# Kernel tuning notes

Hardware: AMD Instinct MI355X
Metric: run time of the kernel (lower is better)

The kernel has to match this reference:

```python
import jax, jax.numpy as jnp
import numpy as np

S, H, E, N, K, R, NL, L = 256, 768, 1536, 16, 4, 48, 2, 1024


def setup_inputs() -> dict:
    key = jax.random.key(0)
    ks = jax.random.split(key, 12)
    def rn(k, shape, s=0.02):
        return jax.random.normal(k, shape, jnp.float32) * s
    return {
        "x": jax.random.normal(ks[0], (L, S), jnp.float32),
        "emb_w": rn(ks[1], (H, S)),
        "emb_b": rn(ks[2], (H,)),
        "norm_w": jnp.ones((NL, H), jnp.float32),
        "in_proj_w": rn(ks[3], (NL, 2 * E, H)),
        "conv_w": rn(ks[4], (NL, E, K), 0.1),
        "conv_b": rn(ks[5], (NL, E), 0.1),
        "x_proj_w": rn(ks[6], (NL, R + 2 * N, E)),
        "dt_proj_w": rn(ks[7], (NL, E, R), 0.1),
        "dt_proj_b": rn(ks[8], (NL, E), 0.1),
        "A_log": jnp.log(jnp.tile(jnp.arange(1, N + 1, dtype=jnp.float32), (NL, E, 1))),
        "D": jnp.ones((NL, E), jnp.float32),
        "out_proj_w": rn(ks[9], (NL, H, E)),
        "head_w": rn(ks[10], (S, H)),
        "head_b": rn(ks[11], (S,)),
    }


def rmsnorm(x, w, eps=1e-5):
    return x * jax.lax.rsqrt(jnp.mean(x * x, axis=-1, keepdims=True) + eps) * w


def causal_conv1d(x, w, b):
    # x: (L, E), w: (E, K) depthwise kernel, causal (left-pad K-1)
    xp = jnp.pad(x, ((K - 1, 0), (0, 0)))
    y = sum(w[:, k] * xp[k:k + x.shape[0]] for k in range(K))
    return y + b


def mamba_mixer(x, in_w, cw, cb, xp_w, dt_w, dt_b, a_log, d, out_w):
    xz = x @ in_w.T                       # (L, 2E)
    xin, z = jnp.split(xz, 2, axis=-1)
    u = jax.nn.silu(causal_conv1d(xin, cw, cb))   # (L, E)
    dbc = u @ xp_w.T                      # (L, R+2N)
    dt, B, C = dbc[:, :R], dbc[:, R:R + N], dbc[:, R + N:]
    dt = jax.nn.softplus(dt @ dt_w.T + dt_b)      # (L, E)
    A = -jnp.exp(a_log)                   # (E, N)
    dA = jnp.exp(dt[:, :, None] * A)      # (L, E, N)
    dBu = dt[:, :, None] * B[:, None, :] * u[:, :, None]  # (L, E, N)

    def step(s, t):
        dA_t, dBu_t, C_t = t
        s = s * dA_t + dBu_t              # (E, N)
        return s, s @ C_t                 # y_t: (E,)

    _, ys = jax.lax.scan(step, jnp.zeros((E, N), x.dtype), (dA, dBu, C))
    y = ys + u * d
    return (y * jax.nn.silu(z)) @ out_w.T


def reference(x, emb_w, emb_b, norm_w, in_proj_w, conv_w, conv_b, x_proj_w,
              dt_proj_w, dt_proj_b, A_log, D, out_proj_w, head_w, head_b):
    h = x @ emb_w.T + emb_b               # (L, H)
    res = None
    for i in range(NL):
        res = h if res is None else h + res
        hn = rmsnorm(res, norm_w[i])
        h = mamba_mixer(hn, in_proj_w[i], conv_w[i], conv_b[i], x_proj_w[i],
                        dt_proj_w[i], dt_proj_b[i], A_log[i], D[i], out_proj_w[i])
    return h @ head_w.T + head_b          # (L, S)
```

## Files before the change

### kernel.cpp

```cpp
#include <hip/hip_runtime.h>
#include <hip/hip_bf16.h>
#include <math.h>

#define SDIM 256
#define HDIM 768
#define EDIM 1536
#define NDIM 16
#define KCONV 4
#define RDIM 48
#define NLAYER 2
#define LSEQ 1024

#define NCHUNK 128
#define CHLEN (LSEQ / NCHUNK)
#define XSPLIT 4
#define XKCH (EDIM / XSPLIT)

typedef __hip_bfloat16 bf16;
typedef __attribute__((ext_vector_type(8))) short short8;
typedef __attribute__((ext_vector_type(4))) float f32x4;

__device__ __forceinline__ float softplusf(float x) {
    return (x > 20.f) ? x : log1pf(expf(x));
}
__device__ __forceinline__ float siluf(float x) {
    return x / (1.f + expf(-x));
}

struct F2BSegs {
    const float* src[6];
    bf16*        dst[6];
    int          n[6];
};

__global__ __launch_bounds__(256) void f2b_all(F2BSegs segs)
{
    for (int s = 0; s < 6; s++) {
        const float* __restrict__ in = segs.src[s];
        bf16* __restrict__ out = segs.dst[s];
        const int n = segs.n[s];
        for (int i = (blockIdx.x * 256 + threadIdx.x) * 4; i < n; i += gridDim.x * 256 * 4) {
            float4 v = *(const float4*)(in + i);
            out[i + 0] = (bf16)v.x; out[i + 1] = (bf16)v.y;
            out[i + 2] = (bf16)v.z; out[i + 3] = (bf16)v.w;
        }
    }
}

__global__ __launch_bounds__(256) void k_gemm_sk(const bf16* __restrict__ A, int lda,
                                                 const bf16* __restrict__ W, int ldw,
                                                 const float* __restrict__ bias,
                                                 float* __restrict__ part,
                                                 int N, int Kh, int useBias)
{
    __shared__ __align__(16) short As[64][72];
    __shared__ __align__(16) short Ws[64][72];

    const int tid  = threadIdx.x;
    const int lane = tid & 63, wid = tid >> 6;
    const int wm = wid >> 1, wn = wid & 1;
    const int row0 = blockIdx.y * 64, col0 = blockIdx.x * 64;
    const int quad = lane >> 4, l16 = lane & 15;
    const int kbase = blockIdx.z * Kh;

    f32x4 acc[2][2] = {};
    for (int k0 = 0; k0 < Kh; k0 += 64) {
        #pragma unroll
        for (int i = 0; i < 2; i++) {
            int id = tid + i * 256;
            int r = id >> 3, g = id & 7;
            *(uint4*)&As[r][g * 8] = *(const uint4*)(A + (size_t)(row0 + r) * lda + kbase + k0 + g * 8);
            *(uint4*)&Ws[r][g * 8] = *(const uint4*)(W + (size_t)(col0 + r) * ldw + kbase + k0 + g * 8);
        }
        __syncthreads();
        #pragma unroll
        for (int ks = 0; ks < 64; ks += 32) {
            short8 af[2], bfr[2];
            #pragma unroll
            for (int i = 0; i < 2; i++) af[i] = *(const short8*)&As[wm * 32 + i * 16 + l16][ks + quad * 8];
            #pragma unroll
            for (int j = 0; j < 2; j++) bfr[j] = *(const short8*)&Ws[wn * 32 + j * 16 + l16][ks + quad * 8];
            #pragma unroll
            for (int i = 0; i < 2; i++)
                #pragma unroll
                for (int j = 0; j < 2; j++)
                    acc[i][j] = __builtin_amdgcn_mfma_f32_16x16x32_bf16(af[i], bfr[j], acc[i][j], 0, 0, 0);
        }
        __syncthreads();
    }
    float* pdst = part + (size_t)blockIdx.z * LSEQ * N;
    #pragma unroll
    for (int i = 0; i < 2; i++) {
        #pragma unroll
        for (int j = 0; j < 2; j++) {
            int gn = col0 + wn * 32 + j * 16 + l16;
            int gm0 = row0 + wm * 32 + i * 16 + quad * 4;
            #pragma unroll
            for (int r = 0; r < 4; r++) {
                float v = acc[i][j][r];
                if (useBias && blockIdx.z == 0) v += bias[gn];
                pdst[(size_t)(gm0 + r) * N + gn] = v;
            }
        }
    }
}

__global__ __launch_bounds__(256) void k_gemm_h(const float* __restrict__ A0,
                                                const float* __restrict__ A1, int lda,
                                                const bf16* __restrict__ W, int ldw,
                                                const float* __restrict__ bias,
                                                float* __restrict__ out, int N, int Kd)
{
    __shared__ __align__(16) short As[64][72];
    __shared__ __align__(16) short Ws[64][72];

    const int tid  = threadIdx.x;
    const int lane = tid & 63, wid = tid >> 6;
    const int wm = wid >> 1, wn = wid & 1;
    const int row0 = blockIdx.y * 64, col0 = blockIdx.x * 64;
    const int quad = lane >> 4, l16 = lane & 15;

    f32x4 acc[2][2] = {};
    for (int k0 = 0; k0 < Kd; k0 += 64) {
        #pragma unroll
        for (int i = 0; i < 2; i++) {
            int id = tid + i * 256;
            int r = id >> 3, g = id & 7;
            size_t base = (size_t)(row0 + r) * lda + k0 + g * 8;
            float4 a0 = *(const float4*)(A0 + base);
            float4 a1 = *(const float4*)(A0 + base + 4);
            float4 b0 = *(const float4*)(A1 + base);
            float4 b1 = *(const float4*)(A1 + base + 4);
            bf16 tmp[8] = {(bf16)(a0.x + b0.x), (bf16)(a0.y + b0.y),
                           (bf16)(a0.z + b0.z), (bf16)(a0.w + b0.w),
                           (bf16)(a1.x + b1.x), (bf16)(a1.y + b1.y),
                           (bf16)(a1.z + b1.z), (bf16)(a1.w + b1.w)};
            *(uint4*)&As[r][g * 8] = *(const uint4*)tmp;
            *(uint4*)&Ws[r][g * 8] = *(const uint4*)(W + (size_t)(col0 + r) * ldw + k0 + g * 8);
        }
        __syncthreads();
        #pragma unroll
        for (int ks = 0; ks < 64; ks += 32) {
            short8 af[2], bfr[2];
            #pragma unroll
            for (int i = 0; i < 2; i++) af[i] = *(const short8*)&As[wm * 32 + i * 16 + l16][ks + quad * 8];
            #pragma unroll
            for (int j = 0; j < 2; j++) bfr[j] = *(const short8*)&Ws[wn * 32 + j * 16 + l16][ks + quad * 8];
            #pragma unroll
            for (int i = 0; i < 2; i++)
                #pragma unroll
                for (int j = 0; j < 2; j++)
                    acc[i][j] = __builtin_amdgcn_mfma_f32_16x16x32_bf16(af[i], bfr[j], acc[i][j], 0, 0, 0);
        }
        __syncthreads();
    }
    #pragma unroll
    for (int i = 0; i < 2; i++) {
        #pragma unroll
        for (int j = 0; j < 2; j++) {
            int gn = col0 + wn * 32 + j * 16 + l16;
            int gm0 = row0 + wm * 32 + i * 16 + quad * 4;
            #pragma unroll
            for (int r = 0; r < 4; r++)
                out[(size_t)(gm0 + r) * N + gn] = acc[i][j][r] + bias[gn];
        }
    }
}

__global__ __launch_bounds__(256) void k_gemm128(
    const bf16* __restrict__ A, int lda,
    const bf16* __restrict__ W, int ldw,
    float* __restrict__ out, int N, int Kd)
{
    __shared__ __align__(16) short As[128][64];
    __shared__ __align__(16) short Ws[128][64];

    const int tid  = threadIdx.x;
    const int lane = tid & 63, wid = tid >> 6;
    const int wm = wid >> 1, wn = wid & 1;
    const int row0 = blockIdx.y * 128, col0 = blockIdx.x * 128;
    const int quad = lane >> 4, l16 = lane & 15;
    const int lr = lane >> 3;
    const int lk = ((lane & 7) ^ lr) * 8;

    f32x4 acc[4][4] = {};

    for (int k0 = 0; k0 < Kd; k0 += 64) {
        #pragma unroll
        for (int j = 0; j < 4; j++) {
            int rg = (wid * 4 + j) * 8;
            const bf16* ga = A + (size_t)(row0 + rg + lr) * lda + k0 + lk;
            const bf16* gw = W + (size_t)(col0 + rg + lr) * ldw + k0 + lk;
            __builtin_amdgcn_global_load_lds(
                (const __attribute__((address_space(1))) void*)ga,
                (__attribute__((address_space(3))) void*)&As[rg][0], 16, 0, 0);
            __builtin_amdgcn_global_load_lds(
                (const __attribute__((address_space(1))) void*)gw,
                (__attribute__((address_space(3))) void*)&Ws[rg][0], 16, 0, 0);
        }
        __syncthreads();

        #pragma unroll
        for (int ks = 0; ks < 64; ks += 32) {
            const int g = (ks >> 3) + quad;
            short8 af[4], bfr[4];
            #pragma unroll
            for (int i = 0; i < 4; i++) {
                int r = wm * 64 + i * 16 + l16;
                af[i] = *(const short8*)&As[r][(g ^ (r & 7)) * 8];
            }
            #pragma unroll
            for (int j = 0; j < 4; j++) {
                int r = wn * 64 + j * 16 + l16;
                bfr[j] = *(const short8*)&Ws[r][(g ^ (r & 7)) * 8];
            }
            #pragma unroll
            for (int i = 0; i < 4; i++)
                #pragma unroll
                for (int j = 0; j < 4; j++)
                    acc[i][j] = __builtin_amdgcn_mfma_f32_16x16x32_bf16(af[i], bfr[j], acc[i][j], 0, 0, 0);
        }
        __syncthreads();
    }

    #pragma unroll
    for (int i = 0; i < 4; i++) {
        #pragma unroll
        for (int j = 0; j < 4; j++) {
            int gn = col0 + wn * 64 + j * 16 + l16;
            int gm0 = row0 + wm * 64 + i * 16 + quad * 4;
            #pragma unroll
            for (int r = 0; r < 4; r++)
                out[(size_t)(gm0 + r) * N + gn] = acc[i][j][r];
        }
    }
}

__global__ __launch_bounds__(256) void k_conv(const float* __restrict__ xz,
                                              const float* __restrict__ cw,
                                              const float* __restrict__ cb,
                                              float* __restrict__ u,
                                              bf16* __restrict__ ub)
{
    const int NG = LSEQ * EDIM / 4;
    for (int g = blockIdx.x * 256 + threadIdx.x; g < NG; g += gridDim.x * 256) {
        int t = g / (EDIM / 4);
        int e4 = (g - t * (EDIM / 4)) * 4;
        float4 s = *(const float4*)(cb + e4);
        #pragma unroll
        for (int k = 0; k < KCONV; k++) {
            int tt = t - (KCONV - 1) + k;
            if (tt >= 0) {
                float4 xv = *(const float4*)(xz + (size_t)tt * (2 * EDIM) + e4);
                s.x += cw[(e4 + 0) * KCONV + k] * xv.x;
                s.y += cw[(e4 + 1) * KCONV + k] * xv.y;
                s.z += cw[(e4 + 2) * KCONV + k] * xv.z;
                s.w += cw[(e4 + 3) * KCONV + k] * xv.w;
            }
        }
        float4 uv;
        uv.x = siluf(s.x); uv.y = siluf(s.y); uv.z = siluf(s.z); uv.w = siluf(s.w);
        size_t o = (size_t)t * EDIM + e4;
        *(float4*)(u + o) = uv;
        bf16 tmp[4] = {(bf16)uv.x, (bf16)uv.y, (bf16)uv.z, (bf16)uv.w};
        *(uint2*)(ub + o) = *(const uint2*)tmp;
    }
}

__global__ __launch_bounds__(256) void k_xproj_mfma(
    const bf16* __restrict__ A,
    const bf16* __restrict__ W,
    float* __restrict__ part)
{
    __shared__ __align__(16) short As[64][72];
    __shared__ __align__(16) short Ws[64][72];

    const int tid  = threadIdx.x;
    const int lane = tid & 63, wid = tid >> 6;
    const int wm = wid >> 1, wn = wid & 1;
    const int row0 = blockIdx.y * 64, col0 = blockIdx.x * 64;
    const int quad = lane >> 4, l16 = lane & 15;
    const int kbase = blockIdx.z * XKCH;

    f32x4 acc[2][2] = {};
    for (int k0 = 0; k0 < XKCH; k0 += 64) {
        #pragma unroll
        for (int i = 0; i < 2; i++) {
            int id = tid + i * 256;
            int r = id >> 3, g = id & 7;
            *(uint4*)&As[r][g * 8] =
                *(const uint4*)(A + (size_t)(row0 + r) * EDIM + kbase + k0 + g * 8);
            uint4 wv = {0, 0, 0, 0};
            if (col0 + r < 80)
                wv = *(const uint4*)(W + (size_t)(col0 + r) * EDIM + kbase + k0 + g * 8);
            *(uint4*)&Ws[r][g * 8] = wv;
        }
        __syncthreads();
        #pragma unroll
        for (int ks = 0; ks < 64; ks += 32) {
            short8 af[2], bfr[2];
            #pragma unroll
            for (int i = 0; i < 2; i++) af[i] = *(const short8*)&As[wm * 32 + i * 16 + l16][ks + quad * 8];
            #pragma unroll
            for (int j = 0; j < 2; j++) bfr[j] = *(const short8*)&Ws[wn * 32 + j * 16 + l16][ks + quad * 8];
            #pragma unroll
            for (int i = 0; i < 2; i++)
                #pragma unroll
                for (int j = 0; j < 2; j++)
                    acc[i][j] = __builtin_amdgcn_mfma_f32_16x16x32_bf16(af[i], bfr[j], acc[i][j], 0, 0, 0);
        }
        __syncthreads();
    }

    float* pdst = part + (size_t)blockIdx.z * (LSEQ * 80);
    #pragma unroll
    for (int i = 0; i < 2; i++) {
        #pragma unroll
        for (int j = 0; j < 2; j++) {
            int gn = col0 + wn * 32 + j * 16 + l16;
            int gm0 = row0 + wm * 32 + i * 16 + quad * 4;
            if (gn < 80) {
                #pragma unroll
                for (int r = 0; r < 4; r++)
                    pdst[(size_t)(gm0 + r) * 80 + gn] = acc[i][j][r];
            }
        }
    }
}

__global__ __launch_bounds__(256) void k_dt_red(
    const float* __restrict__ part, const float* __restrict__ dtw,
    const float* __restrict__ dtbb, float* __restrict__ out,
    float* __restrict__ dbc)
{
    __shared__ float AsF[16][68];
    __shared__ float WsF[16][68];
    const int tid = threadIdx.x;
    const int tx = tid & 15, ty = tid >> 4;
    const int tx4 = tx * 4, ty4 = ty * 4;
    const int row0 = blockIdx.y * 64, col0 = blockIdx.x * 64;

    if (blockIdx.x == 0) {
        for (int idx = tid; idx < 64 * 32; idx += 256) {
            int m = idx >> 5, c = 48 + (idx & 31);
            size_t o = (size_t)(row0 + m) * 80 + c;
            float s = 0.f;
            #pragma unroll
            for (int p = 0; p < XSPLIT; p++) s += part[(size_t)p * (LSEQ * 80) + o];
            dbc[o] = s;
        }
    }

    float acc[4][4] = {};
    for (int k0 = 0; k0 < RDIM; k0 += 16) {
        #pragma unroll
        for (int i = 0; i < 4; i++) {
            int idx = tid + i * 256;
            int m = idx >> 4, kk = idx & 15;
            size_t o = (size_t)(row0 + m) * 80 + k0 + kk;
            float s = 0.f;
            #pragma unroll
            for (int p = 0; p < XSPLIT; p++) s += part[(size_t)p * (LSEQ * 80) + o];
            AsF[kk][m] = s;
        }
        #pragma unroll
        for (int i = 0; i < 4; i++) {
            int idx = tid + i * 256;
            int nn = idx >> 4, kk = idx & 15;
            WsF[kk][nn] = dtw[(size_t)(col0 + nn) * RDIM + k0 + kk];
        }
        __syncthreads();
        #pragma unroll
        for (int kk = 0; kk < 16; kk++) {
            float av[4], bv[4];
            #pragma unroll
            for (int i = 0; i < 4; i++) av[i] = AsF[kk][ty4 + i];
            #pragma unroll
            for (int j = 0; j < 4; j++) bv[j] = WsF[kk][tx4 + j];
            #pragma unroll
            for (int i = 0; i < 4; i++)
                #pragma unroll
                for (int j = 0; j < 4; j++)
                    acc[i][j] += av[i] * bv[j];
        }
        __syncthreads();
    }
    #pragma unroll
    for (int i = 0; i < 4; i++) {
        int gm = row0 + ty4 + i;
        #pragma unroll
        for (int j = 0; j < 4; j++) {
            int gn = col0 + tx4 + j;
            float v = acc[i][j] + dtbb[gn];
            out[(size_t)gm * EDIM + gn] = softplusf(v);
        }
    }
}

__global__ __launch_bounds__(256) void k_rms(const float* __restrict__ h0,
                                             const float* __restrict__ h1,
                                             float* __restrict__ res,
                                             bf16* __restrict__ hnb, const float* __restrict__ w,
                                             int first)
{
    __shared__ float red[4];
    __shared__ float tot;
    const int tid = threadIdx.x;
    const int t = blockIdx.x;
    float v[3]; float ss = 0.f;
    #pragma unroll
    for (int r = 0; r < 3; r++) {
        int j = tid + r * 256;
        float xv = h0[(size_t)t * HDIM + j] + h1[(size_t)t * HDIM + j];
        if (!first) xv += res[(size_t)t * HDIM + j];
        v[r] = xv;
        res[(size_t)t * HDIM + j] = xv;
        ss += xv * xv;
    }
    #pragma unroll
    for (int m = 32; m >= 1; m >>= 1) ss += __shfl_down(ss, m);
    int wid = tid >> 6;
    if ((tid & 63) == 0) red[wid] = ss;
    __syncthreads();
    if (tid == 0) tot = red[0] + red[1] + red[2] + red[3];
    __syncthreads();
    float scale = rsqrtf(tot / (float)HDIM + 1e-5f);
    #pragma unroll
    for (int r = 0; r < 3; r++) {
        int j = tid + r * 256;
        hnb[(size_t)t * HDIM + j] = (bf16)(v[r] * scale * w[j]);
    }
}

__global__ __launch_bounds__(256) void k_scan1(const float* __restrict__ dt,
                                               const float* __restrict__ u,
                                               const float* __restrict__ dbc,
                                               const float* __restrict__ a_log,
                                               float* __restrict__ chunkS,
                                               float* __restrict__ sumdt)
{
    const int ex = blockIdx.x % 6, c = blockIdx.x / 6;
    const int e = ex * 256 + threadIdx.x;
    float A[16];
    #pragma unroll
    for (int q = 0; q < 4; q++) {
        float4 a4 = *(const float4*)(a_log + e * NDIM + q * 4);
        A[q*4+0] = -__expf(a4.x); A[q*4+1] = -__expf(a4.y);
        A[q*4+2] = -__expf(a4.z); A[q*4+3] = -__expf(a4.w);
    }
    float s[16] = {};
    float sd = 0.f;
    const int t0 = c * CHLEN;
    #pragma unroll
    for (int tt = 0; tt < CHLEN; tt++) {
        int t = t0 + tt;
        float dtv = dt[(size_t)t * EDIM + e];
        float uv  = u[(size_t)t * EDIM + e];
        float dtu = dtv * uv;
        sd += dtv;
        float4 B4[4];
        #pragma unroll
        for (int q = 0; q < 4; q++) B4[q] = *(const float4*)(dbc + (size_t)t * 80 + RDIM + q * 4);
        const float* B = (const float*)B4;
        #pragma unroll
        for (int n = 0; n < 16; n++) s[n] = s[n] * __expf(dtv * A[n]) + dtu * B[n];
    }
    float* cs = chunkS + ((size_t)c * EDIM + e) * NDIM;
    #pragma unroll
    for (int q = 0; q < 4; q++)
        *(float4*)(cs + q * 4) = make_float4(s[q*4+0], s[q*4+1], s[q*4+2], s[q*4+3]);
    sumdt[(size_t)c * EDIM + e] = sd;
}

__global__ __launch_bounds__(256) void k_scan2(const float* __restrict__ chunkS,
                                               const float* __restrict__ sumdt,
                                               const float* __restrict__ a_log,
                                               float* __restrict__ sInit)
{
    int gid = blockIdx.x * 256 + threadIdx.x;
    if (gid >= EDIM * NDIM) return;
    int n = gid & 15, e = gid >> 4;
    const float Aen = -__expf(a_log[gid]);
    float s = 0.f;
    for (int c = 0; c < NCHUNK; c++) {
        sInit[((size_t)c * EDIM + e) * NDIM + n] = s;
        float P = __expf(Aen * sumdt[(size_t)c * EDIM + e]);
        s = s * P + chunkS[((size_t)c * EDIM + e) * NDIM + n];
    }
}

__global__ __launch_bounds__(256) void k_scan3(const float* __restrict__ dt,
                                               const float* __restrict__ u,
                                               const float* __restrict__ dbc,
                                               const float* __restrict__ xz,
                                               const float* __restrict__ a_log,
                                               const float* __restrict__ Dp,
                                               const float* __restrict__ sInit,
                                               bf16* __restrict__ yzb)
{
    const int ex = blockIdx.x % 6, c = blockIdx.x / 6;
    const int e = ex * 256 + threadIdx.x;
    float A[16];
    #pragma unroll
    for (int q = 0; q < 4; q++) {
        float4 a4 = *(const float4*)(a_log + e * NDIM + q * 4);
        A[q*4+0] = -__expf(a4.x); A[q*4+1] = -__expf(a4.y);
        A[q*4+2] = -__expf(a4.z); A[q*4+3] = -__expf(a4.w);
    }
    const float dv = Dp[e];
    float s[16];
    const float* si = sInit + ((size_t)c * EDIM + e) * NDIM;
    #pragma unroll
    for (int q = 0; q < 4; q++) {
        float4 s4 = *(const float4*)(si + q * 4);
        s[q*4+0] = s4.x; s[q*4+1] = s4.y; s[q*4+2] = s4.z; s[q*4+3] = s4.w;
    }
    const int t0 = c * CHLEN;
    #pragma unroll
    for (int tt = 0; tt < CHLEN; tt++) {
        int t = t0 + tt;
        float dtv = dt[(size_t)t * EDIM + e];
        float uv  = u[(size_t)t * EDIM + e];
        float zv  = xz[(size_t)t * (2 * EDIM) + EDIM + e];
        float dtu = dtv * uv;
        float4 B4[4], C4[4];
        #pragma unroll
        for (int q = 0; q < 4; q++) {
            B4[q] = *(const float4*)(dbc + (size_t)t * 80 + RDIM + q * 4);
            C4[q] = *(const float4*)(dbc + (size_t)t * 80 + RDIM + NDIM + q * 4);
        }
        const float* B = (const float*)B4;
        const float* C = (const float*)C4;
        float y = 0.f;
        #pragma unroll
        for (int n = 0; n < 16; n++) {
            s[n] = s[n] * __expf(dtv * A[n]) + dtu * B[n];
            y += s[n] * C[n];
        }
        y += uv * dv;
        yzb[(size_t)t * EDIM + e] = (bf16)(y * siluf(zv));
    }
}

extern "C" void kernel_launch(void* const* d_in, const int* in_sizes, int n_in,
                              void* d_out, int out_size, void* d_ws, size_t ws_size,
                              hipStream_t stream)
{
    const float* x        = (const float*)d_in[0];
    const float* emb_w    = (const float*)d_in[1];
    const float* emb_b    = (const float*)d_in[2];
    const float* norm_w   = (const float*)d_in[3];
    const float* in_proj  = (const float*)d_in[4];
    const float* conv_w   = (const float*)d_in[5];
    const float* conv_b   = (const float*)d_in[6];
    const float* x_proj   = (const float*)d_in[7];
    const float* dt_w     = (const float*)d_in[8];
    const float* dt_b     = (const float*)d_in[9];
    const float* A_log    = (const float*)d_in[10];
    const float* Dp       = (const float*)d_in[11];
    const float* out_proj = (const float*)d_in[12];
    const float* head_w   = (const float*)d_in[13];
    const float* head_b   = (const float*)d_in[14];
    float* out = (float*)d_out;

    float* ws = (float*)d_ws;
    size_t off = 0;
    float* hpart  = ws + off; off += (size_t)2 * LSEQ * HDIM;
    float* res    = ws + off; off += (size_t)LSEQ * HDIM;
    float* xz     = ws + off; off += (size_t)LSEQ * 2 * EDIM;
    float* u      = ws + off; off += (size_t)LSEQ * EDIM;
    float* dbc    = ws + off; off += (size_t)LSEQ * 80;
    float* part   = ws + off; off += (size_t)XSPLIT * LSEQ * 80;
    float* dtb    = ws + off; off += (size_t)LSEQ * EDIM;
    float* chunkS = ws + off; off += (size_t)NCHUNK * EDIM * NDIM;
    float* sumdt  = ws + off; off += (size_t)NCHUNK * EDIM;
    float* sInit  = ws + off; off += (size_t)NCHUNK * EDIM * NDIM;
    bf16* hnb     = (bf16*)(ws + off); off += (size_t)LSEQ * HDIM / 2;
    bf16* yzb     = (bf16*)(ws + off); off += (size_t)LSEQ * EDIM / 2;
    bf16* ub      = (bf16*)(ws + off); off += (size_t)LSEQ * EDIM / 2;
    bf16* xb      = (bf16*)(ws + off); off += (size_t)LSEQ * SDIM / 2;
    bf16* emb_wb  = (bf16*)(ws + off); off += (size_t)HDIM * SDIM / 2;
    bf16* head_wb = (bf16*)(ws + off); off += (size_t)SDIM * HDIM / 2;
    bf16* in_wb   = (bf16*)(ws + off); off += (size_t)NLAYER * 2 * EDIM * HDIM / 2;
    bf16* out_wb  = (bf16*)(ws + off); off += (size_t)NLAYER * HDIM * EDIM / 2;
    bf16* xwb     = (bf16*)(ws + off); off += (size_t)NLAYER * 80 * EDIM / 2;

    F2BSegs segs;
    segs.src[0] = x;        segs.dst[0] = xb;      segs.n[0] = LSEQ * SDIM;
    segs.src[1] = emb_w;    segs.dst[1] = emb_wb;  segs.n[1] = HDIM * SDIM;
    segs.src[2] = head_w;   segs.dst[2] = head_wb; segs.n[2] = SDIM * HDIM;
    segs.src[3] = in_proj;  segs.dst[3] = in_wb;   segs.n[3] = NLAYER * 2 * EDIM * HDIM;
    segs.src[4] = out_proj; segs.dst[4] = out_wb;  segs.n[4] = NLAYER * HDIM * EDIM;
    segs.src[5] = x_proj;   segs.dst[5] = xwb;     segs.n[5] = NLAYER * 80 * EDIM;
    f2b_all<<<1024, 256, 0, stream>>>(segs);

    k_gemm_sk<<<dim3(12, 16, 2), 256, 0, stream>>>(xb, SDIM, emb_wb, SDIM, emb_b,
                                                   hpart, HDIM, SDIM / 2, 1);

    for (int l = 0; l < NLAYER; l++) {
        const bf16*  inw  = in_wb  + (size_t)l * 2 * EDIM * HDIM;
        const bf16*  outw = out_wb + (size_t)l * HDIM * EDIM;
        const bf16*  xwbl = xwb    + (size_t)l * 80 * EDIM;
        const float* cw   = conv_w + (size_t)l * EDIM * KCONV;
        const float* cb   = conv_b + (size_t)l * EDIM;
        const float* dtw  = dt_w   + (size_t)l * EDIM * RDIM;
        const float* dtbb = dt_b   + (size_t)l * EDIM;
        const float* al   = A_log  + (size_t)l * EDIM * NDIM;
        const float* Dpl  = Dp     + (size_t)l * EDIM;

        k_rms<<<LSEQ, 256, 0, stream>>>(hpart, hpart + (size_t)LSEQ * HDIM, res,
                                        hnb, norm_w + (size_t)l * HDIM, l == 0);
        k_gemm128<<<dim3(24, 8), 256, 0, stream>>>(hnb, HDIM, inw, HDIM,
                                                   xz, 2 * EDIM, HDIM);
        k_conv<<<1536, 256, 0, stream>>>(xz, cw, cb, u, ub);
        k_xproj_mfma<<<dim3(2, 16, XSPLIT), 256, 0, stream>>>(ub, xwbl, part);
        k_dt_red<<<dim3(24, 16), 256, 0, stream>>>(part, dtw, dtbb, dtb, dbc);
        k_scan1<<<6 * NCHUNK, 256, 0, stream>>>(dtb, u, dbc, al, chunkS, sumdt);
        k_scan2<<<96, 256, 0, stream>>>(chunkS, sumdt, al, sInit);
        k_scan3<<<6 * NCHUNK, 256, 0, stream>>>(dtb, u, dbc, xz, al, Dpl, sInit, yzb);
        k_gemm_sk<<<dim3(12, 16, 2), 256, 0, stream>>>(yzb, EDIM, outw, EDIM, nullptr,
                                                       hpart, HDIM, EDIM / 2, 0);
    }

    k_gemm_h<<<dim3(4, 16), 256, 0, stream>>>(hpart, hpart + (size_t)LSEQ * HDIM, HDIM,
                                              head_wb, HDIM, head_b, out, SDIM, HDIM);
}
```

Before: 375.7 us.

## Split-K in_proj GEMM, drop fp32 u buffer, halve scan chunk count

The dedicated 128x128 in_proj GEMM is replaced by the split-K GEMM kernel. It writes two partial xz buffers, which the conv and scan3 kernels sum when they read them. The fp32 u activation is no longer stored, and the scans read the bf16 copy instead, cutting memory traffic at some cost in precision. The scan chunk count drops from 128 to 64 with partial unrolling, which reduces chunk-state traffic but lengthens each serial chunk.

```diff
diff --git a/kernel.cpp b/kernel.cpp
--- a/kernel.cpp
+++ b/kernel.cpp
@@ -11,7 +11,7 @@
 #define NLAYER 2
 #define LSEQ 1024
 
-#define NCHUNK 128
+#define NCHUNK 64
 #define CHLEN (LSEQ / NCHUNK)
 #define XSPLIT 4
 #define XKCH (EDIM / XSPLIT)
@@ -167,79 +167,10 @@
     }
 }
 
-__global__ __launch_bounds__(256) void k_gemm128(
-    const bf16* __restrict__ A, int lda,
-    const bf16* __restrict__ W, int ldw,
-    float* __restrict__ out, int N, int Kd)
-{
-    __shared__ __align__(16) short As[128][64];
-    __shared__ __align__(16) short Ws[128][64];
-
-    const int tid  = threadIdx.x;
-    const int lane = tid & 63, wid = tid >> 6;
-    const int wm = wid >> 1, wn = wid & 1;
-    const int row0 = blockIdx.y * 128, col0 = blockIdx.x * 128;
-    const int quad = lane >> 4, l16 = lane & 15;
-    const int lr = lane >> 3;
-    const int lk = ((lane & 7) ^ lr) * 8;
-
-    f32x4 acc[4][4] = {};
-
-    for (int k0 = 0; k0 < Kd; k0 += 64) {
-        #pragma unroll
-        for (int j = 0; j < 4; j++) {
-            int rg = (wid * 4 + j) * 8;
-            const bf16* ga = A + (size_t)(row0 + rg + lr) * lda + k0 + lk;
-            const bf16* gw = W + (size_t)(col0 + rg + lr) * ldw + k0 + lk;
-            __builtin_amdgcn_global_load_lds(
-                (const __attribute__((address_space(1))) void*)ga,
-                (__attribute__((address_space(3))) void*)&As[rg][0], 16, 0, 0);
-            __builtin_amdgcn_global_load_lds(
-                (const __attribute__((address_space(1))) void*)gw,
-                (__attribute__((address_space(3))) void*)&Ws[rg][0], 16, 0, 0);
-        }
-        __syncthreads();
-
-        #pragma unroll
-        for (int ks = 0; ks < 64; ks += 32) {
-            const int g = (ks >> 3) + quad;
-            short8 af[4], bfr[4];
-            #pragma unroll
-            for (int i = 0; i < 4; i++) {
-                int r = wm * 64 + i * 16 + l16;
-                af[i] = *(const short8*)&As[r][(g ^ (r & 7)) * 8];
-            }
-            #pragma unroll
-            for (int j = 0; j < 4; j++) {
-                int r = wn * 64 + j * 16 + l16;
-                bfr[j] = *(const short8*)&Ws[r][(g ^ (r & 7)) * 8];
-            }
-            #pragma unroll
-            for (int i = 0; i < 4; i++)
-                #pragma unroll
-                for (int j = 0; j < 4; j++)
-                    acc[i][j] = __builtin_amdgcn_mfma_f32_16x16x32_bf16(af[i], bfr[j], acc[i][j], 0, 0, 0);
-        }
-        __syncthreads();
-    }
-
-    #pragma unroll
-    for (int i = 0; i < 4; i++) {
-        #pragma unroll
-        for (int j = 0; j < 4; j++) {
-            int gn = col0 + wn * 64 + j * 16 + l16;
-            int gm0 = row0 + wm * 64 + i * 16 + quad * 4;
-            #pragma unroll
-            for (int r = 0; r < 4; r++)
-                out[(size_t)(gm0 + r) * N + gn] = acc[i][j][r];
-        }
-    }
-}
-
-__global__ __launch_bounds__(256) void k_conv(const float* __restrict__ xz,
+__global__ __launch_bounds__(256) void k_conv(const float* __restrict__ xzp0,
+                                              const float* __restrict__ xzp1,
                                               const float* __restrict__ cw,
                                               const float* __restrict__ cb,
-                                              float* __restrict__ u,
                                               bf16* __restrict__ ub)
 {
     const int NG = LSEQ * EDIM / 4;
@@ -251,19 +182,17 @@
         for (int k = 0; k < KCONV; k++) {
             int tt = t - (KCONV - 1) + k;
             if (tt >= 0) {
-                float4 xv = *(const float4*)(xz + (size_t)tt * (2 * EDIM) + e4);
-                s.x += cw[(e4 + 0) * KCONV + k] * xv.x;
-                s.y += cw[(e4 + 1) * KCONV + k] * xv.y;
-                s.z += cw[(e4 + 2) * KCONV + k] * xv.z;
-                s.w += cw[(e4 + 3) * KCONV + k] * xv.w;
+                size_t o = (size_t)tt * (2 * EDIM) + e4;
+                float4 xa = *(const float4*)(xzp0 + o);
+                float4 xb2 = *(const float4*)(xzp1 + o);
+                s.x += cw[(e4 + 0) * KCONV + k] * (xa.x + xb2.x);
+                s.y += cw[(e4 + 1) * KCONV + k] * (xa.y + xb2.y);
+                s.z += cw[(e4 + 2) * KCONV + k] * (xa.z + xb2.z);
+                s.w += cw[(e4 + 3) * KCONV + k] * (xa.w + xb2.w);
             }
         }
-        float4 uv;
-        uv.x = siluf(s.x); uv.y = siluf(s.y); uv.z = siluf(s.z); uv.w = siluf(s.w);
-        size_t o = (size_t)t * EDIM + e4;
-        *(float4*)(u + o) = uv;
-        bf16 tmp[4] = {(bf16)uv.x, (bf16)uv.y, (bf16)uv.z, (bf16)uv.w};
-        *(uint2*)(ub + o) = *(const uint2*)tmp;
+        bf16 tmp[4] = {(bf16)siluf(s.x), (bf16)siluf(s.y), (bf16)siluf(s.z), (bf16)siluf(s.w)};
+        *(uint2*)(ub + (size_t)t * EDIM + e4) = *(const uint2*)tmp;
     }
 }
 
@@ -433,7 +362,7 @@
 }
 
 __global__ __launch_bounds__(256) void k_scan1(const float* __restrict__ dt,
-                                               const float* __restrict__ u,
+                                               const bf16* __restrict__ ub,
                                                const float* __restrict__ dbc,
                                                const float* __restrict__ a_log,
                                                float* __restrict__ chunkS,
@@ -451,11 +380,11 @@
     float s[16] = {};
     float sd = 0.f;
     const int t0 = c * CHLEN;
-    #pragma unroll
+    #pragma unroll 2
     for (int tt = 0; tt < CHLEN; tt++) {
         int t = t0 + tt;
         float dtv = dt[(size_t)t * EDIM + e];
-        float uv  = u[(size_t)t * EDIM + e];
+        float uv  = (float)ub[(size_t)t * EDIM + e];
         float dtu = dtv * uv;
         sd += dtv;
         float4 B4[4];
@@ -490,9 +419,10 @@
 }
 
 __global__ __launch_bounds__(256) void k_scan3(const float* __restrict__ dt,
-                                               const float* __restrict__ u,
+                                               const bf16* __restrict__ ub,
                                                const float* __restrict__ dbc,
-                                               const float* __restrict__ xz,
+                                               const float* __restrict__ xzp0,
+                                               const float* __restrict__ xzp1,
                                                const float* __restrict__ a_log,
                                                const float* __restrict__ Dp,
                                                const float* __restrict__ sInit,
@@ -516,12 +446,13 @@
         s[q*4+0] = s4.x; s[q*4+1] = s4.y; s[q*4+2] = s4.z; s[q*4+3] = s4.w;
     }
     const int t0 = c * CHLEN;
-    #pragma unroll
+    #pragma unroll 2
     for (int tt = 0; tt < CHLEN; tt++) {
         int t = t0 + tt;
         float dtv = dt[(size_t)t * EDIM + e];
-        float uv  = u[(size_t)t * EDIM + e];
-        float zv  = xz[(size_t)t * (2 * EDIM) + EDIM + e];
+        float uv  = (float)ub[(size_t)t * EDIM + e];
+        size_t zo = (size_t)t * (2 * EDIM) + EDIM + e;
+        float zv  = xzp0[zo] + xzp1[zo];
         float dtu = dtv * uv;
         float4 B4[4], C4[4];
         #pragma unroll
@@ -566,9 +497,8 @@
     float* ws = (float*)d_ws;
     size_t off = 0;
     float* hpart  = ws + off; off += (size_t)2 * LSEQ * HDIM;
+    float* xzpart = ws + off; off += (size_t)2 * LSEQ * 2 * EDIM;
     float* res    = ws + off; off += (size_t)LSEQ * HDIM;
-    float* xz     = ws + off; off += (size_t)LSEQ * 2 * EDIM;
-    float* u      = ws + off; off += (size_t)LSEQ * EDIM;
     float* dbc    = ws + off; off += (size_t)LSEQ * 80;
     float* part   = ws + off; off += (size_t)XSPLIT * LSEQ * 80;
     float* dtb    = ws + off; off += (size_t)LSEQ * EDIM;
@@ -610,14 +540,17 @@
 
         k_rms<<<LSEQ, 256, 0, stream>>>(hpart, hpart + (size_t)LSEQ * HDIM, res,
                                         hnb, norm_w + (size_t)l * HDIM, l == 0);
-        k_gemm128<<<dim3(24, 8), 256, 0, stream>>>(hnb, HDIM, inw, HDIM,
-                                                   xz, 2 * EDIM, HDIM);
-        k_conv<<<1536, 256, 0, stream>>>(xz, cw, cb, u, ub);
+        k_gemm_sk<<<dim3(48, 16, 2), 256, 0, stream>>>(hnb, HDIM, inw, HDIM, nullptr,
+                                                       xzpart, 2 * EDIM, HDIM / 2, 0);
+        k_conv<<<1536, 256, 0, stream>>>(xzpart, xzpart + (size_t)LSEQ * 2 * EDIM,
+                                         cw, cb, ub);
         k_xproj_mfma<<<dim3(2, 16, XSPLIT), 256, 0, stream>>>(ub, xwbl, part);
         k_dt_red<<<dim3(24, 16), 256, 0, stream>>>(part, dtw, dtbb, dtb, dbc);
-        k_scan1<<<6 * NCHUNK, 256, 0, stream>>>(dtb, u, dbc, al, chunkS, sumdt);
+        k_scan1<<<6 * NCHUNK, 256, 0, stream>>>(dtb, ub, dbc, al, chunkS, sumdt);
         k_scan2<<<96, 256, 0, stream>>>(chunkS, sumdt, al, sInit);
-        k_scan3<<<6 * NCHUNK, 256, 0, stream>>>(dtb, u, dbc, xz, al, Dpl, sInit, yzb);
+        k_scan3<<<6 * NCHUNK, 256, 0, stream>>>(dtb, ub, dbc,
+                                                xzpart, xzpart + (size_t)LSEQ * 2 * EDIM,
+                                                al, Dpl, sInit, yzb);
         k_gemm_sk<<<dim3(12, 16, 2), 256, 0, stream>>>(yzb, EDIM, outw, EDIM, nullptr,
                                                        hpart, HDIM, EDIM / 2, 0);
     }
```

Result: no change. 372.6 us (-0.8%).
